# Performance work log

Hardware: AMD Instinct MI355X
Metric: run time of the kernel (lower is better)

The kernel has to match this reference:

```python
import jax, jax.numpy as jnp
import numpy as np

B, N, D = 2, 256, 128
LN_EPS = 1e-5


def _linear_params(key, d, scale):
    kw, kb = jax.random.split(key)
    W = jax.random.normal(kw, (d, d), jnp.float32) * scale
    b = jax.random.normal(kb, (d,), jnp.float32) * 0.02
    return W, b


def setup_inputs() -> dict:
    key = jax.random.key(0)
    ks = jax.random.split(key, 8)
    hidden_states = jax.random.normal(ks[0], (B, N, D), jnp.float32)
    structure_matrix = jax.random.normal(ks[1], (B, N, N, D), jnp.float32)
    scale = 1.0 / np.sqrt(D).astype(np.float32)
    Wq, bq = _linear_params(ks[2], D, scale)
    Wk, bk = _linear_params(ks[3], D, scale)
    Wv, bv = _linear_params(ks[4], D, scale)
    Wo, bo = _linear_params(ks[5], D, scale)
    ln_g = jnp.ones((D,), jnp.float32)
    ln_b = jnp.zeros((D,), jnp.float32)
    return dict(hidden_states=hidden_states, structure_matrix=structure_matrix,
                Wq=Wq, bq=bq, Wk=Wk, bk=bk, Wv=Wv, bv=bv, Wo=Wo, bo=bo,
                ln_g=ln_g, ln_b=ln_b)


def reference(hidden_states, structure_matrix, Wq, bq, Wk, bk, Wv, bv, Wo, bo, ln_g, ln_b):
    # hidden_states is accepted by the original forward but never used.
    d = structure_matrix.shape[-1]
    q = structure_matrix @ Wq + bq  # [B,N,N,D]
    k = structure_matrix @ Wk + bk
    v = structure_matrix @ Wv + bv
    # scores[b,i,j,k] = <Q[b,i,k,:], K[b,i,j,:]> / sqrt(D)
    # (equivalent to the torch broadcast multiply+sum, expressed as batched GEMM)
    scores = jnp.einsum('bikd,bijd->bijk', q, k) / jnp.sqrt(jnp.asarray(d, scores_dtype := q.dtype))
    probs = jax.nn.relu(scores)  # dropout is identity in eval mode
    # context[b,i,j,d] = sum_k probs[b,i,j,k] * V[b,i,k,d]
    ctx = jnp.einsum('bijk,bikd->bijd', probs, v)
    out = ctx @ Wo + bo
    x = out + structure_matrix  # residual
    mu = jnp.mean(x, axis=-1, keepdims=True)
    var = jnp.var(x, axis=-1, keepdims=True)
    return (x - mu) * jax.lax.rsqrt(var + LN_EPS) * ln_g + ln_b
```

## Files before the change

kernel.cpp:

```cpp
#include <hip/hip_runtime.h>

#define DEV static __device__ __forceinline__

typedef __bf16 bf16x8 __attribute__((ext_vector_type(8)));
typedef float  f32x16 __attribute__((ext_vector_type(16)));

DEV int rowmap(int r, int hi) { return (r & 3) + 8 * (r >> 2) + 4 * hi; }

DEV int swzQ(int row, int col) {
  return row * 256 + (((((col >> 3) ^ (row & 15)) << 3) | (col & 7)) << 1);
}
DEV int swzV(int d, int k) {
  return d * 512 + (((((k >> 3) ^ (d & 31)) << 3) | (k & 7)) << 1);
}

DEV unsigned pack2(float lo, float hi) {
  union { __bf16 h[2]; unsigned u; } x;
  x.h[0] = (__bf16)lo; x.h[1] = (__bf16)hi;
  return x.u;
}

DEV bf16x8 mk_frag(float d0, float d1, float d2, float d3,
                   float d4, float d5, float d6, float d7, int lane) {
  unsigned a0 = pack2(d0, d1), a1 = pack2(d2, d3);
  unsigned b0 = pack2(d4, d5), b1 = pack2(d6, d7);
  unsigned a0s = __shfl_xor(a0, 32), a1s = __shfl_xor(a1, 32);
  unsigned b0s = __shfl_xor(b0, 32), b1s = __shfl_xor(b1, 32);
  bool lo = lane < 32;
  union { unsigned u[4]; bf16x8 v; } r;
  r.u[0] = lo ? a0  : b0s;
  r.u[1] = lo ? a1  : b1s;
  r.u[2] = lo ? a0s : b0;
  r.u[3] = lo ? a1s : b1;
  return r.v;
}

DEV f32x16 fzero() {
  f32x16 z;
  #pragma unroll
  for (int i = 0; i < 16; ++i) z[i] = 0.f;
  return z;
}

DEV void gld16(const char* g, char* l) {
  __builtin_amdgcn_global_load_lds(
      (const __attribute__((address_space(1))) void*)g,
      (__attribute__((address_space(3))) void*)l, 16, 0, 0);
}

DEV void stage_w32(const float* __restrict__ W, char* dst, int tid) {
  #pragma unroll
  for (int it = 0; it < 32; ++it) {
    int idx = tid + it * 512;
    int e = idx >> 7, dp = idx & 127;
    *reinterpret_cast<__bf16*>(dst + swzQ(dp, e)) = (__bf16)W[idx];
  }
}

__global__ void prep_wt(const float* __restrict__ Wk, const float* __restrict__ Wq,
                        const float* __restrict__ Wv, const float* __restrict__ Wo,
                        __bf16* __restrict__ wt) {
  int idx = blockIdx.x * 256 + threadIdx.x;
  const float* W[4] = {Wk, Wq, Wv, Wo};
  int m = idx >> 14, rem = idx & 16383;
  int e = rem >> 7, dp = rem & 127;
  wt[m * 16384 + (swzQ(dp, e) >> 1)] = (__bf16)W[m][rem];
}

template<bool WS>
__global__ __launch_bounds__(512, 2)
void sapd_fused(const float* __restrict__ S,
                const float* __restrict__ bq, const float* __restrict__ bk,
                const float* __restrict__ bv, const float* __restrict__ bo,
                const float* __restrict__ Wq, const float* __restrict__ Wk,
                const float* __restrict__ Wv, const float* __restrict__ Wo,
                const float* __restrict__ lg, const float* __restrict__ lb,
                const __bf16* __restrict__ wt,
                float* __restrict__ out)
{
  extern __shared__ char smem[];
  char* QL = smem;
  char* VT = smem + 65536;

  const int tid  = threadIdx.x;
  const int lane = tid & 63;
  const int w    = tid >> 6;
  const int ml   = lane & 31;
  const int hi   = lane >> 5;
  const size_t sbase = (size_t)blockIdx.x * (256 * 128);
  const char* wsc = (const char*)wt;

  if (WS) {
    #pragma unroll
    for (int j = 0; j < 12; ++j) {
      int c = w + 8 * j;
      char* dst = (c < 64) ? (VT + c * 1024) : (QL + (c - 64) * 1024);
      gld16(wsc + c * 1024 + lane * 16, dst);
    }
  } else {
    stage_w32(Wk, VT, tid);
    stage_w32(Wq, VT + 32768, tid);
    stage_w32(Wv, QL, tid);
  }

  bf16x8 sfrag[8];
  {
    const float* srow = S + sbase + (size_t)(32 * w + ml) * 128;
    #pragma unroll
    for (int kk = 0; kk < 8; ++kk) {
      float4 a = *reinterpret_cast<const float4*>(srow + 16 * kk + 8 * hi);
      float4 b = *reinterpret_cast<const float4*>(srow + 16 * kk + 8 * hi + 4);
      bf16x8 f;
      f[0] = (__bf16)a.x; f[1] = (__bf16)a.y; f[2] = (__bf16)a.z; f[3] = (__bf16)a.w;
      f[4] = (__bf16)b.x; f[5] = (__bf16)b.y; f[6] = (__bf16)b.z; f[7] = (__bf16)b.w;
      sfrag[kk] = f;
    }
  }
  __syncthreads();

  f32x16 accK[4];
  #pragma unroll
  for (int t = 0; t < 4; ++t) accK[t] = fzero();
  #pragma unroll
  for (int kk = 0; kk < 8; ++kk) {
    #pragma unroll
    for (int t = 0; t < 4; ++t) {
      bf16x8 wf = *reinterpret_cast<const bf16x8*>(
          VT + swzQ(32 * t + ml, 16 * kk + 8 * hi));
      accK[t] = __builtin_amdgcn_mfma_f32_32x32x16_bf16(wf, sfrag[kk], accK[t], 0, 0, 0);
    }
  }
  bf16x8 kfrag[8];
  #pragma unroll
  for (int t = 0; t < 4; ++t) {
    #pragma unroll
    for (int r = 0; r < 16; ++r) accK[t][r] += bk[32 * t + rowmap(r, hi)];
    kfrag[2 * t]     = mk_frag(accK[t][0], accK[t][1], accK[t][2], accK[t][3],
                               accK[t][4], accK[t][5], accK[t][6], accK[t][7], lane);
    kfrag[2 * t + 1] = mk_frag(accK[t][8], accK[t][9], accK[t][10], accK[t][11],
                               accK[t][12], accK[t][13], accK[t][14], accK[t][15], lane);
  }

  f32x16 accQ[4];
  #pragma unroll
  for (int t = 0; t < 4; ++t) accQ[t] = fzero();
  #pragma unroll
  for (int kk = 0; kk < 8; ++kk) {
    #pragma unroll
    for (int t = 0; t < 4; ++t) {
      bf16x8 wf = *reinterpret_cast<const bf16x8*>(
          VT + 32768 + swzQ(32 * t + ml, 16 * kk + 8 * hi));
      accQ[t] = __builtin_amdgcn_mfma_f32_32x32x16_bf16(sfrag[kk], wf, accQ[t], 0, 0, 0);
    }
  }

  f32x16 accV[4];
  #pragma unroll
  for (int t = 0; t < 4; ++t) accV[t] = fzero();
  #pragma unroll
  for (int kk = 0; kk < 8; ++kk) {
    #pragma unroll
    for (int t = 0; t < 4; ++t) {
      bf16x8 wf = *reinterpret_cast<const bf16x8*>(
          QL + swzQ(32 * t + ml, 16 * kk + 8 * hi));
      accV[t] = __builtin_amdgcn_mfma_f32_32x32x16_bf16(sfrag[kk], wf, accV[t], 0, 0, 0);
    }
  }
  __syncthreads();

  #pragma unroll
  for (int t = 0; t < 4; ++t) {
    float bb = bq[32 * t + ml];
    #pragma unroll
    for (int r = 0; r < 16; ++r)
      *reinterpret_cast<__bf16*>(
          QL + swzQ(32 * w + rowmap(r, hi), 32 * t + ml)) =
          (__bf16)(accQ[t][r] + bb);
  }
  #pragma unroll
  for (int t = 0; t < 4; ++t) {
    float bb = bv[32 * t + ml];
    int d = 32 * t + ml;
    #pragma unroll
    for (int p = 0; p < 8; ++p) {
      int k = 32 * w + rowmap(2 * p, hi);
      *reinterpret_cast<unsigned*>(VT + swzV(d, k)) =
          pack2(accV[t][2 * p] + bb, accV[t][2 * p + 1] + bb);
    }
  }
  __syncthreads();

  f32x16 ctx[4];
  #pragma unroll
  for (int m = 0; m < 4; ++m) ctx[m] = fzero();
  const float SC = 0.088388347648318447f;

  #pragma unroll 4
  for (int kt = 0; kt < 8; ++kt) {
    f32x16 sa = fzero();
    #pragma unroll
    for (int kk = 0; kk < 8; ++kk) {
      bf16x8 qf = *reinterpret_cast<const bf16x8*>(
          QL + swzQ(32 * kt + ml, 16 * kk + 8 * hi));
      sa = __builtin_amdgcn_mfma_f32_32x32x16_bf16(qf, kfrag[kk], sa, 0, 0, 0);
    }
    float p[16];
    #pragma unroll
    for (int r = 0; r < 16; ++r) p[r] = fmaxf(sa[r] * SC, 0.f);
    bf16x8 pf0 = mk_frag(p[0], p[1], p[2], p[3], p[4], p[5], p[6], p[7], lane);
    bf16x8 pf1 = mk_frag(p[8], p[9], p[10], p[11], p[12], p[13], p[14], p[15], lane);
    #pragma unroll
    for (int m = 0; m < 4; ++m) {
      bf16x8 vf0 = *reinterpret_cast<const bf16x8*>(
          VT + swzV(32 * m + ml, 32 * kt + 8 * hi));
      ctx[m] = __builtin_amdgcn_mfma_f32_32x32x16_bf16(vf0, pf0, ctx[m], 0, 0, 0);
      bf16x8 vf1 = *reinterpret_cast<const bf16x8*>(
          VT + swzV(32 * m + ml, 32 * kt + 16 + 8 * hi));
      ctx[m] = __builtin_amdgcn_mfma_f32_32x32x16_bf16(vf1, pf1, ctx[m], 0, 0, 0);
    }
  }

  bf16x8 cf[8];
  #pragma unroll
  for (int m = 0; m < 4; ++m) {
    cf[2 * m]     = mk_frag(ctx[m][0], ctx[m][1], ctx[m][2], ctx[m][3],
                            ctx[m][4], ctx[m][5], ctx[m][6], ctx[m][7], lane);
    cf[2 * m + 1] = mk_frag(ctx[m][8], ctx[m][9], ctx[m][10], ctx[m][11],
                            ctx[m][12], ctx[m][13], ctx[m][14], ctx[m][15], lane);
  }
  __syncthreads();
  if (WS) {
    #pragma unroll
    for (int j = 0; j < 4; ++j) {
      int c = w + 8 * j;
      gld16(wsc + 98304 + c * 1024 + lane * 16, QL + c * 1024);
    }
  } else {
    stage_w32(Wo, QL, tid);
  }
  float resv[4][16];
  #pragma unroll
  for (int t = 0; t < 4; ++t) {
    #pragma unroll
    for (int r = 0; r < 16; ++r)
      resv[t][r] = S[sbase + (size_t)(32 * w + rowmap(r, hi)) * 128 + 32 * t + ml];
  }
  __syncthreads();

  f32x16 oa[4];
  #pragma unroll
  for (int t = 0; t < 4; ++t) oa[t] = fzero();
  #pragma unroll
  for (int kk = 0; kk < 8; ++kk) {
    #pragma unroll
    for (int t = 0; t < 4; ++t) {
      bf16x8 wf = *reinterpret_cast<const bf16x8*>(
          QL + swzQ(32 * t + ml, 16 * kk + 8 * hi));
      oa[t] = __builtin_amdgcn_mfma_f32_32x32x16_bf16(cf[kk], wf, oa[t], 0, 0, 0);
    }
  }

  float gg[4], lbv[4], bov[4];
  #pragma unroll
  for (int t = 0; t < 4; ++t) {
    gg[t]  = lg[32 * t + ml];
    lbv[t] = lb[32 * t + ml];
    bov[t] = bo[32 * t + ml];
  }
  float sum[16], ssq[16];
  #pragma unroll
  for (int r = 0; r < 16; ++r) { sum[r] = 0.f; ssq[r] = 0.f; }
  #pragma unroll
  for (int t = 0; t < 4; ++t) {
    #pragma unroll
    for (int r = 0; r < 16; ++r) {
      float x = oa[t][r] + bov[t] + resv[t][r];
      oa[t][r] = x;
      sum[r] += x;
      ssq[r] += x * x;
    }
  }
  #pragma unroll
  for (int r = 0; r < 16; ++r) {
    float s_ = sum[r], q_ = ssq[r];
    #pragma unroll
    for (int m = 1; m <= 16; m <<= 1) {
      s_ += __shfl_xor(s_, m);
      q_ += __shfl_xor(q_, m);
    }
    float mu = s_ * (1.f / 128.f);
    float var = q_ * (1.f / 128.f) - mu * mu;
    float rs = rsqrtf(var + 1e-5f);
    float* orow = out + sbase + (size_t)(32 * w + rowmap(r, hi)) * 128;
    #pragma unroll
    for (int t = 0; t < 4; ++t)
      orow[32 * t + ml] = (oa[t][r] - mu) * rs * gg[t] + lbv[t];
  }
}

extern "C" void kernel_launch(void* const* d_in, const int* in_sizes, int n_in,
                              void* d_out, int out_size, void* d_ws, size_t ws_size,
                              hipStream_t stream) {
  (void)in_sizes; (void)n_in; (void)out_size;
  const float* S  = (const float*)d_in[1];
  const float* Wq = (const float*)d_in[2];
  const float* bq = (const float*)d_in[3];
  const float* Wk = (const float*)d_in[4];
  const float* bk = (const float*)d_in[5];
  const float* Wv = (const float*)d_in[6];
  const float* bv = (const float*)d_in[7];
  const float* Wo = (const float*)d_in[8];
  const float* bo = (const float*)d_in[9];
  const float* lg = (const float*)d_in[10];
  const float* lb = (const float*)d_in[11];
  float* out = (float*)d_out;

  constexpr int SMEM = 131072;
  bool use_ws = (d_ws != nullptr) && (ws_size >= 131072);
  if (use_ws) {
    prep_wt<<<dim3(256), dim3(256), 0, stream>>>(Wk, Wq, Wv, Wo, (__bf16*)d_ws);
    (void)hipFuncSetAttribute(reinterpret_cast<const void*>(&sapd_fused<true>),
                              hipFuncAttributeMaxDynamicSharedMemorySize, SMEM);
    sapd_fused<true><<<dim3(512), dim3(512), SMEM, stream>>>(
        S, bq, bk, bv, bo, Wq, Wk, Wv, Wo, lg, lb, (const __bf16*)d_ws, out);
  } else {
    (void)hipFuncSetAttribute(reinterpret_cast<const void*>(&sapd_fused<false>),
                              hipFuncAttributeMaxDynamicSharedMemorySize, SMEM);
    sapd_fused<false><<<dim3(512), dim3(512), SMEM, stream>>>(
        S, bq, bk, bv, bo, Wq, Wk, Wv, Wo, lg, lb, nullptr, out);
  }
}
```

Measured before the change: 73.76 us.

## Reorder K/V/Q projections to cut live registers and prefetch Wo mid-loop

Computes K, then V, then Q in scoped blocks so only one projection accumulator is live at a time. V is written to its LDS region after an extra barrier, and Q goes into the other region. The Wo weight load is issued halfway through the attention loop (after kt==3), once the first half of the Q rows has been consumed, so it overlaps with the remaining MFMA work. The change also adds s_setprio around the MFMA bursts and lowers the attention-loop unroll from 4 to 2. The added barriers and the mid-loop sync may cost time in exchange for lower register pressure and the overlapped load.

Result: no change. 72.79 us (-1.3%).

```diff
diff --git a/kernel.cpp b/kernel.cpp
--- a/kernel.cpp
+++ b/kernel.cpp
@@ -79,8 +79,8 @@
                 float* __restrict__ out)
 {
   extern __shared__ char smem[];
-  char* QL = smem;
-  char* VT = smem + 65536;
+  char* RA = smem;
+  char* RB = smem + 65536;
 
   const int tid  = threadIdx.x;
   const int lane = tid & 63;
@@ -94,13 +94,13 @@
     #pragma unroll
     for (int j = 0; j < 12; ++j) {
       int c = w + 8 * j;
-      char* dst = (c < 64) ? (VT + c * 1024) : (QL + (c - 64) * 1024);
+      char* dst = (c < 64) ? (RB + c * 1024) : (RA + (c - 64) * 1024);
       gld16(wsc + c * 1024 + lane * 16, dst);
     }
   } else {
-    stage_w32(Wk, VT, tid);
-    stage_w32(Wq, VT + 32768, tid);
-    stage_w32(Wv, QL, tid);
+    stage_w32(Wk, RB, tid);
+    stage_w32(Wq, RB + 32768, tid);
+    stage_w32(Wv, RA, tid);
   }
 
   bf16x8 sfrag[8];
@@ -118,74 +118,80 @@
   }
   __syncthreads();
 
-  f32x16 accK[4];
-  #pragma unroll
-  for (int t = 0; t < 4; ++t) accK[t] = fzero();
-  #pragma unroll
-  for (int kk = 0; kk < 8; ++kk) {
+  bf16x8 kfrag[8];
+  {
+    f32x16 accK[4];
+    #pragma unroll
+    for (int t = 0; t < 4; ++t) accK[t] = fzero();
+    #pragma unroll
+    for (int kk = 0; kk < 8; ++kk) {
+      #pragma unroll
+      for (int t = 0; t < 4; ++t) {
+        bf16x8 wf = *reinterpret_cast<const bf16x8*>(
+            RB + swzQ(32 * t + ml, 16 * kk + 8 * hi));
+        accK[t] = __builtin_amdgcn_mfma_f32_32x32x16_bf16(wf, sfrag[kk], accK[t], 0, 0, 0);
+      }
+    }
     #pragma unroll
     for (int t = 0; t < 4; ++t) {
-      bf16x8 wf = *reinterpret_cast<const bf16x8*>(
-          VT + swzQ(32 * t + ml, 16 * kk + 8 * hi));
-      accK[t] = __builtin_amdgcn_mfma_f32_32x32x16_bf16(wf, sfrag[kk], accK[t], 0, 0, 0);
-    }
-  }
-  bf16x8 kfrag[8];
-  #pragma unroll
-  for (int t = 0; t < 4; ++t) {
-    #pragma unroll
-    for (int r = 0; r < 16; ++r) accK[t][r] += bk[32 * t + rowmap(r, hi)];
-    kfrag[2 * t]     = mk_frag(accK[t][0], accK[t][1], accK[t][2], accK[t][3],
-                               accK[t][4], accK[t][5], accK[t][6], accK[t][7], lane);
-    kfrag[2 * t + 1] = mk_frag(accK[t][8], accK[t][9], accK[t][10], accK[t][11],
-                               accK[t][12], accK[t][13], accK[t][14], accK[t][15], lane);
-  }
-
-  f32x16 accQ[4];
-  #pragma unroll
-  for (int t = 0; t < 4; ++t) accQ[t] = fzero();
-  #pragma unroll
-  for (int kk = 0; kk < 8; ++kk) {
+      #pragma unroll
+      for (int r = 0; r < 16; ++r) accK[t][r] += bk[32 * t + rowmap(r, hi)];
+      kfrag[2 * t]     = mk_frag(accK[t][0], accK[t][1], accK[t][2], accK[t][3],
+                                 accK[t][4], accK[t][5], accK[t][6], accK[t][7], lane);
+      kfrag[2 * t + 1] = mk_frag(accK[t][8], accK[t][9], accK[t][10], accK[t][11],
+                                 accK[t][12], accK[t][13], accK[t][14], accK[t][15], lane);
+    }
+  }
+
+  {
+    f32x16 accV[4];
+    #pragma unroll
+    for (int t = 0; t < 4; ++t) accV[t] = fzero();
+    #pragma unroll
+    for (int kk = 0; kk < 8; ++kk) {
+      #pragma unroll
+      for (int t = 0; t < 4; ++t) {
+        bf16x8 wf = *reinterpret_cast<const bf16x8*>(
+            RA + swzQ(32 * t + ml, 16 * kk + 8 * hi));
+        accV[t] = __builtin_amdgcn_mfma_f32_32x32x16_bf16(sfrag[kk], wf, accV[t], 0, 0, 0);
+      }
+    }
+    __syncthreads();
     #pragma unroll
     for (int t = 0; t < 4; ++t) {
-      bf16x8 wf = *reinterpret_cast<const bf16x8*>(
-          VT + 32768 + swzQ(32 * t + ml, 16 * kk + 8 * hi));
-      accQ[t] = __builtin_amdgcn_mfma_f32_32x32x16_bf16(sfrag[kk], wf, accQ[t], 0, 0, 0);
-    }
-  }
-
-  f32x16 accV[4];
-  #pragma unroll
-  for (int t = 0; t < 4; ++t) accV[t] = fzero();
-  #pragma unroll
-  for (int kk = 0; kk < 8; ++kk) {
+      float bb = bv[32 * t + ml];
+      int d = 32 * t + ml;
+      #pragma unroll
+      for (int p = 0; p < 8; ++p) {
+        int k = 32 * w + rowmap(2 * p, hi);
+        *reinterpret_cast<unsigned*>(RA + swzV(d, k)) =
+            pack2(accV[t][2 * p] + bb, accV[t][2 * p + 1] + bb);
+      }
+    }
+  }
+
+  {
+    f32x16 accQ[4];
+    #pragma unroll
+    for (int t = 0; t < 4; ++t) accQ[t] = fzero();
+    #pragma unroll
+    for (int kk = 0; kk < 8; ++kk) {
+      #pragma unroll
+      for (int t = 0; t < 4; ++t) {
+        bf16x8 wf = *reinterpret_cast<const bf16x8*>(
+            RB + 32768 + swzQ(32 * t + ml, 16 * kk + 8 * hi));
+        accQ[t] = __builtin_amdgcn_mfma_f32_32x32x16_bf16(sfrag[kk], wf, accQ[t], 0, 0, 0);
+      }
+    }
+    __syncthreads();
     #pragma unroll
     for (int t = 0; t < 4; ++t) {
-      bf16x8 wf = *reinterpret_cast<const bf16x8*>(
-          QL + swzQ(32 * t + ml, 16 * kk + 8 * hi));
-      accV[t] = __builtin_amdgcn_mfma_f32_32x32x16_bf16(sfrag[kk], wf, accV[t], 0, 0, 0);
-    }
-  }
-  __syncthreads();
-
-  #pragma unroll
-  for (int t = 0; t < 4; ++t) {
-    float bb = bq[32 * t + ml];
-    #pragma unroll
-    for (int r = 0; r < 16; ++r)
-      *reinterpret_cast<__bf16*>(
-          QL + swzQ(32 * w + rowmap(r, hi), 32 * t + ml)) =
-          (__bf16)(accQ[t][r] + bb);
-  }
-  #pragma unroll
-  for (int t = 0; t < 4; ++t) {
-    float bb = bv[32 * t + ml];
-    int d = 32 * t + ml;
-    #pragma unroll
-    for (int p = 0; p < 8; ++p) {
-      int k = 32 * w + rowmap(2 * p, hi);
-      *reinterpret_cast<unsigned*>(VT + swzV(d, k)) =
-          pack2(accV[t][2 * p] + bb, accV[t][2 * p + 1] + bb);
+      float bb = bq[32 * t + ml];
+      #pragma unroll
+      for (int r = 0; r < 16; ++r)
+        *reinterpret_cast<__bf16*>(
+            RB + swzQ(32 * w + rowmap(r, hi), 32 * t + ml)) =
+            (__bf16)(accQ[t][r] + bb);
     }
   }
   __syncthreads();
@@ -195,28 +201,45 @@
   for (int m = 0; m < 4; ++m) ctx[m] = fzero();
   const float SC = 0.088388347648318447f;
 
-  #pragma unroll 4
+  #pragma unroll 2
   for (int kt = 0; kt < 8; ++kt) {
     f32x16 sa = fzero();
+    __builtin_amdgcn_s_setprio(1);
     #pragma unroll
     for (int kk = 0; kk < 8; ++kk) {
       bf16x8 qf = *reinterpret_cast<const bf16x8*>(
-          QL + swzQ(32 * kt + ml, 16 * kk + 8 * hi));
+          RB + swzQ(32 * kt + ml, 16 * kk + 8 * hi));
       sa = __builtin_amdgcn_mfma_f32_32x32x16_bf16(qf, kfrag[kk], sa, 0, 0, 0);
     }
+    __builtin_amdgcn_s_setprio(0);
     float p[16];
     #pragma unroll
     for (int r = 0; r < 16; ++r) p[r] = fmaxf(sa[r] * SC, 0.f);
     bf16x8 pf0 = mk_frag(p[0], p[1], p[2], p[3], p[4], p[5], p[6], p[7], lane);
     bf16x8 pf1 = mk_frag(p[8], p[9], p[10], p[11], p[12], p[13], p[14], p[15], lane);
+    __builtin_amdgcn_s_setprio(1);
     #pragma unroll
     for (int m = 0; m < 4; ++m) {
       bf16x8 vf0 = *reinterpret_cast<const bf16x8*>(
-          VT + swzV(32 * m + ml, 32 * kt + 8 * hi));
+          RA + swzV(32 * m + ml, 32 * kt + 8 * hi));
       ctx[m] = __builtin_amdgcn_mfma_f32_32x32x16_bf16(vf0, pf0, ctx[m], 0, 0, 0);
       bf16x8 vf1 = *reinterpret_cast<const bf16x8*>(
-          VT + swzV(32 * m + ml, 32 * kt + 16 + 8 * hi));
+          RA + swzV(32 * m + ml, 32 * kt + 16 + 8 * hi));
       ctx[m] = __builtin_amdgcn_mfma_f32_32x32x16_bf16(vf1, pf1, ctx[m], 0, 0, 0);
+    }
+    __builtin_amdgcn_s_setprio(0);
+
+    if (kt == 3) {
+      __syncthreads();
+      if (WS) {
+        #pragma unroll
+        for (int j = 0; j < 4; ++j) {
+          int c = w + 8 * j;
+          gld16(wsc + 98304 + c * 1024 + lane * 16, RB + c * 1024);
+        }
+      } else {
+        stage_w32(Wo, RB, tid);
+      }
     }
   }
 
@@ -228,16 +251,6 @@
     cf[2 * m + 1] = mk_frag(ctx[m][8], ctx[m][9], ctx[m][10], ctx[m][11],
                             ctx[m][12], ctx[m][13], ctx[m][14], ctx[m][15], lane);
   }
-  __syncthreads();
-  if (WS) {
-    #pragma unroll
-    for (int j = 0; j < 4; ++j) {
-      int c = w + 8 * j;
-      gld16(wsc + 98304 + c * 1024 + lane * 16, QL + c * 1024);
-    }
-  } else {
-    stage_w32(Wo, QL, tid);
-  }
   float resv[4][16];
   #pragma unroll
   for (int t = 0; t < 4; ++t) {
@@ -255,7 +268,7 @@
     #pragma unroll
     for (int t = 0; t < 4; ++t) {
       bf16x8 wf = *reinterpret_cast<const bf16x8*>(
-          QL + swzQ(32 * t + ml, 16 * kk + 8 * hi));
+          RB + swzQ(32 * t + ml, 16 * kk + 8 * hi));
       oa[t] = __builtin_amdgcn_mfma_f32_32x32x16_bf16(cf[kk], wf, oa[t], 0, 0, 0);
     }
   }
```
